# Optimization experiments

Measured on AMD Instinct MI355X. Metric: run time of the kernel, lower is better.

## Reference

```python
import jax, jax.numpy as jnp
import numpy as np

C = 8.0


def setup_inputs() -> dict:
    key = jax.random.key(0)
    k1, k2, k3, k4 = jax.random.split(key, 4)
    B, H, W = 16, 512, 512
    grid = jax.random.normal(k1, (B, 2, H, W), jnp.float32)
    u = jax.random.uniform(k2, (B, 2), jnp.float32)
    # dx = -C*x takes both signs (exercise both branches); dy = C*y >= 0 as the
    # original torch slicing requires.
    gt_sym_axis = jnp.stack([u[:, 0] * 2.0 - 1.0, u[:, 1]], axis=-1)
    gd_sym_axis = jax.random.normal(k3, (B, 2), jnp.float32)
    mask = jax.random.uniform(k4, (B, H, W), jnp.float32)
    return {"grid": grid, "gt_sym_axis": gt_sym_axis,
            "gd_sym_axis": gd_sym_axis, "mask": mask}


def _per_item(g, m, dx, dy, sym_x, sym_y):
    # g: (2, H, W) flow grid, m: (H, W) mask; dx, dy, sym_x, sym_y scalars.
    _, h, w = g.shape
    dy1f = jnp.floor(dy); dx1f = jnp.floor(dx)
    dy2f = dy1f + 1.0;    dx2f = dx1f + 1.0
    dy1 = dy1f.astype(jnp.int32); dy2 = dy1 + 1
    dx1 = dx1f.astype(jnp.int32); dx2 = dx1 + 1

    ii = jnp.arange(h)[:, None]   # (H, 1)
    jj = jnp.arange(w)[None, :]   # (1, W)

    def gat(arr, r, c):
        # clipped dynamic gather; invalid region is masked out later
        return arr[..., jnp.clip(r, 0, h - 1), jnp.clip(c, 0, w - 1)]

    wcol = {1: dx2f - dx, 2: dx - dx1f}   # bilinear col weights (dx1 / dx2)
    wrow = {1: dy2f - dy, 2: dy - dy1f}   # bilinear row weights (dy1 / dy2)
    dys = {1: dy1, 2: dy2}
    dxs = {1: dx1, 2: dx2}

    # ---- dx > 0 branch: delta_ba(i,j) = g[i,j] - g[i+dy_a, j+dx_b] ----
    delta_p = jnp.zeros_like(g)
    for b in (1, 2):
        for a in (1, 2):
            delta_p = delta_p + wcol[b] * wrow[a] * (g - gat(g, ii + dys[a], jj + dxs[b]))
    valid_p = ((ii < h - dy2) & (jj < w - dx2)).astype(g.dtype)
    err_p = delta_p[0] * sym_y + delta_p[1] * sym_x
    cnt_p = ((h - dy2) * (w - dx2)).astype(g.dtype)
    loss_p = jnp.sum(m * valid_p * err_p * err_p) / cnt_p

    # ---- dx <= 0 branch: delta_ba(i,j) = g[i+dy2, j+t_b] - g[i+s_a, j+t_b-dx_b] ----
    s = {1: 1, 2: 0}   # row base offset for dy1 / dy2 variant
    t = {1: 0, 2: 1}   # col base offset for dx1 / dx2 variant
    delta_n = jnp.zeros_like(g)
    for b in (1, 2):
        for a in (1, 2):
            first = gat(g, ii + dy2, jj + t[b])
            second = gat(g, ii + s[a], jj + t[b] - dxs[b])
            delta_n = delta_n + wcol[b] * wrow[a] * (first - second)
    valid_n = ((ii < h - dy2) & (jj < w + dx1)).astype(g.dtype)
    m_n = gat(m, ii + dy2, jj - dx1)
    err_n = delta_n[0] * sym_y + delta_n[1] * sym_x
    cnt_n = ((h - dy2) * (w + dx1)).astype(g.dtype)
    loss_n = jnp.sum(m_n * valid_n * err_n * err_n) / cnt_n

    return jnp.where(dx > 0, loss_p, loss_n)


def reference(grid, gt_sym_axis, gd_sym_axis, mask):
    dx = -C * gt_sym_axis[:, 0]
    dy = C * gt_sym_axis[:, 1]
    sym_x = gd_sym_axis[:, 0]
    sym_y = gd_sym_axis[:, 1]
    losses = jax.vmap(_per_item)(grid, mask, dx, dy, sym_x, sym_y)
    return jnp.mean(losses)
```

## Files before the change

### kernel.cpp

```cpp
#include <hip/hip_runtime.h>

#define HH 512
#define WW 512
#define NB 16
#define NRB 2
#define NCHUNK (HH / NRB)
#define NBLOCKS (NB * NCHUNK)

__device__ __forceinline__ int swz(int c) { return ((c & 3) << 7) | (c >> 2); }

__global__ __launch_bounds__(256) void mbfs_main(
    const float* __restrict__ grid,
    const float* __restrict__ gt,
    const float* __restrict__ gd,
    const float* __restrict__ mask,
    float* __restrict__ partials)
{
    __shared__ float lds[6 * 512];

    const int b    = blockIdx.y;
    const int i0   = blockIdx.x * NRB;
    const int tid  = threadIdx.x;
    const int rsub = tid >> 7;
    const int jt   = tid & 127;
    const int j0   = jt << 2;

    const float dx   = -8.0f * gt[2 * b + 0];
    const float dy   =  8.0f * gt[2 * b + 1];
    const float symx = gd[2 * b + 0];
    const float symy = gd[2 * b + 1];

    const float dy1f = floorf(dy);
    const float dx1f = floorf(dx);
    const int dy1 = (int)dy1f;
    const int dx1 = (int)dx1f;
    const int dy2 = dy1 + 1;
    const int dx2 = dx1 + 1;
    const float wc1 = (dx1f + 1.0f) - dx;
    const float wc2 = dx - dx1f;
    const float wr1 = (dy1f + 1.0f) - dy;
    const float wr2 = dy - dy1f;

    const float* g0 = grid + (size_t)b * 2 * HH * WW;
    const float* g1 = g0 + HH * WW;
    const float* mk = mask + (size_t)b * HH * WW;

    const int imax = HH - dy2;
    float acc = 0.0f;
    float cnt;

    if (dx > 0.0f) {
        const int jmax = WW - dx2;
        cnt = (float)imax * (float)jmax;

        for (int t = tid; t < 6 * 128; t += 256) {
            const int s  = t >> 7;
            const int f  = t & 127;
            const int c  = f << 2;
            const int rr = (s < 3) ? s : s - 3;
            const float* gp = (s < 3) ? g0 : g1;
            int ir = min(i0 + dy1 + rr, HH - 1);
            const float4 v = *(const float4*)(gp + ir * WW + c);
            float* L = lds + s * 512;
            L[swz(c)]     = v.x;
            L[swz(c + 1)] = v.y;
            L[swz(c + 2)] = v.z;
            L[swz(c + 3)] = v.w;
        }
        __syncthreads();

        const int i = i0 + rsub;
        if (i < imax) {
            const float4 c0 = *(const float4*)(g0 + i * WW + j0);
            const float4 c1 = *(const float4*)(g1 + i * WW + j0);
            const float4 mv = *(const float4*)(mk + i * WW + j0);
            const float* A0 = lds + rsub * 512;
            const float* B0 = lds + (rsub + 1) * 512;
            const float* A1 = lds + (3 + rsub) * 512;
            const float* B1 = lds + (4 + rsub) * 512;

            float z0[5], z1[5];
            #pragma unroll
            for (int k = 0; k < 5; ++k) {
                const int c  = min(j0 + dx1 + k, WW - 1);
                const int sc = swz(c);
                z0[k] = wr1 * A0[sc] + wr2 * B0[sc];
                z1[k] = wr1 * A1[sc] + wr2 * B1[sc];
            }
            const float cc0[4] = {c0.x, c0.y, c0.z, c0.w};
            const float cc1[4] = {c1.x, c1.y, c1.z, c1.w};
            const float mm[4]  = {mv.x, mv.y, mv.z, mv.w};
            #pragma unroll
            for (int k = 0; k < 4; ++k) {
                const float s0 = wc1 * z0[k] + wc2 * z0[k + 1];
                const float s1 = wc1 * z1[k] + wc2 * z1[k + 1];
                const float d0 = cc0[k] - s0;
                const float d1 = cc1[k] - s1;
                const float e  = d0 * symy + d1 * symx;
                const float w  = (j0 + k < jmax) ? mm[k] : 0.0f;
                acc += w * e * e;
            }
        }
    } else {
        const int a    = -dx1;
        const int jmax = WW + dx1;
        cnt = (float)imax * (float)jmax;

        for (int t = tid; t < 4 * 128; t += 256) {
            const int s  = t >> 7;
            const int f  = t & 127;
            const int c  = f << 2;
            const int rr = s & 1;
            const float* gp = (s < 2) ? g0 : g1;
            int ir = min(i0 + dy2 + rr, HH - 1);
            const float4 v = *(const float4*)(gp + ir * WW + c);
            float* L = lds + s * 512;
            L[swz(c)]     = v.x;
            L[swz(c + 1)] = v.y;
            L[swz(c + 2)] = v.z;
            L[swz(c + 3)] = v.w;
        }
        __syncthreads();

        const int i = i0 + rsub;
        if (i < imax) {
            const float4 p00 = *(const float4*)(g0 + i * WW + j0);
            const float4 p01 = *(const float4*)(g0 + (i + 1) * WW + j0);
            const float4 p10 = *(const float4*)(g1 + i * WW + j0);
            const float4 p11 = *(const float4*)(g1 + (i + 1) * WW + j0);
            const float4 mv  = *(const float4*)(mk + (i + dy2) * WW + j0);
            const float* H0 = lds + rsub * 512;
            const float* H1 = lds + (2 + rsub) * 512;

            float hh0[5], hh1[5];
            #pragma unroll
            for (int k = 0; k < 5; ++k) {
                int c = j0 - a + k;
                c = max(0, min(c, WW - 1));
                const int sc = swz(c);
                hh0[k] = H0[sc];
                hh1[k] = H1[sc];
            }
            const float q00[4] = {p00.x, p00.y, p00.z, p00.w};
            const float q01[4] = {p01.x, p01.y, p01.z, p01.w};
            const float q10[4] = {p10.x, p10.y, p10.z, p10.w};
            const float q11[4] = {p11.x, p11.y, p11.z, p11.w};
            const float mm[4]  = {mv.x, mv.y, mv.z, mv.w};
            #pragma unroll
            for (int k = 0; k < 4; ++k) {
                const float zn0 = wr1 * q01[k] + wr2 * q00[k];
                const float zn1 = wr1 * q11[k] + wr2 * q10[k];
                const float d0  = wc1 * hh0[k] + wc2 * hh0[k + 1] - zn0;
                const float d1  = wc1 * hh1[k] + wc2 * hh1[k + 1] - zn1;
                const float e   = d0 * symy + d1 * symx;
                const float w   = (j0 + k >= a) ? mm[k] : 0.0f;
                acc += w * e * e;
            }
        }
    }

    #pragma unroll
    for (int off = 32; off > 0; off >>= 1)
        acc += __shfl_down(acc, off, 64);
    __shared__ float part[4];
    const int lane = tid & 63;
    const int wv   = tid >> 6;
    if (lane == 0) part[wv] = acc;
    __syncthreads();
    if (tid == 0) {
        const float s = part[0] + part[1] + part[2] + part[3];
        partials[b * NCHUNK + blockIdx.x] = s / (cnt * (float)NB);
    }
}

__global__ __launch_bounds__(256) void mbfs_reduce(
    const float* __restrict__ partials, float* __restrict__ out)
{
    float v = 0.0f;
    for (int idx = threadIdx.x; idx < NBLOCKS; idx += 256) v += partials[idx];
    #pragma unroll
    for (int off = 32; off > 0; off >>= 1)
        v += __shfl_down(v, off, 64);
    __shared__ float part[4];
    const int lane = threadIdx.x & 63;
    const int wv   = threadIdx.x >> 6;
    if (lane == 0) part[wv] = v;
    __syncthreads();
    if (threadIdx.x == 0) out[0] = part[0] + part[1] + part[2] + part[3];
}

extern "C" void kernel_launch(void* const* d_in, const int* in_sizes, int n_in,
                              void* d_out, int out_size, void* d_ws, size_t ws_size,
                              hipStream_t stream) {
    const float* grid_p = (const float*)d_in[0];
    const float* gt_p   = (const float*)d_in[1];
    const float* gd_p   = (const float*)d_in[2];
    const float* mask_p = (const float*)d_in[3];
    float* out_p = (float*)d_out;
    float* ws_p  = (float*)d_ws;

    dim3 g(NCHUNK, NB);
    mbfs_main<<<g, 256, 0, stream>>>(grid_p, gt_p, gd_p, mask_p, ws_p);
    mbfs_reduce<<<1, 256, 0, stream>>>(ws_p, out_p);
}
```

Before: 97.61 us.

## Replace LDS staging with direct aligned vector loads and process four rows per block

Removes the shared-memory staging of shifted rows and the barrier that follows it. Each thread now reads two aligned float4 windows straight from global memory and selects the shifted elements in registers with a runtime offset. In the dx<=0 branch the indexing is re-based so the shifted operand is the contiguous one, and the mask is read at the shifted position. Each block also handles four rows instead of two, which halves the grid. In exchange, global loads become redundant and overlapping, relying on cache hits, and the register-select logic adds ALU work.

```diff
diff --git a/kernel.cpp b/kernel.cpp
--- a/kernel.cpp
+++ b/kernel.cpp
@@ -3,11 +3,9 @@
 #define HH 512
 #define WW 512
 #define NB 16
-#define NRB 2
+#define NRB 4
 #define NCHUNK (HH / NRB)
 #define NBLOCKS (NB * NCHUNK)
-
-__device__ __forceinline__ int swz(int c) { return ((c & 3) << 7) | (c >> 2); }
 
 __global__ __launch_bounds__(256) void mbfs_main(
     const float* __restrict__ grid,
@@ -16,14 +14,11 @@
     const float* __restrict__ mask,
     float* __restrict__ partials)
 {
-    __shared__ float lds[6 * 512];
-
     const int b    = blockIdx.y;
     const int i0   = blockIdx.x * NRB;
     const int tid  = threadIdx.x;
     const int rsub = tid >> 7;
-    const int jt   = tid & 127;
-    const int j0   = jt << 2;
+    const int j0   = (tid & 127) << 2;
 
     const float dx   = -8.0f * gt[2 * b + 0];
     const float dy   =  8.0f * gt[2 * b + 1];
@@ -52,116 +47,140 @@
     if (dx > 0.0f) {
         const int jmax = WW - dx2;
         cnt = (float)imax * (float)jmax;
-
-        for (int t = tid; t < 6 * 128; t += 256) {
-            const int s  = t >> 7;
-            const int f  = t & 127;
-            const int c  = f << 2;
-            const int rr = (s < 3) ? s : s - 3;
-            const float* gp = (s < 3) ? g0 : g1;
-            int ir = min(i0 + dy1 + rr, HH - 1);
-            const float4 v = *(const float4*)(gp + ir * WW + c);
-            float* L = lds + s * 512;
-            L[swz(c)]     = v.x;
-            L[swz(c + 1)] = v.y;
-            L[swz(c + 2)] = v.z;
-            L[swz(c + 3)] = v.w;
-        }
-        __syncthreads();
-
-        const int i = i0 + rsub;
-        if (i < imax) {
-            const float4 c0 = *(const float4*)(g0 + i * WW + j0);
-            const float4 c1 = *(const float4*)(g1 + i * WW + j0);
-            const float4 mv = *(const float4*)(mk + i * WW + j0);
-            const float* A0 = lds + rsub * 512;
-            const float* B0 = lds + (rsub + 1) * 512;
-            const float* A1 = lds + (3 + rsub) * 512;
-            const float* B1 = lds + (4 + rsub) * 512;
-
-            float z0[5], z1[5];
-            #pragma unroll
-            for (int k = 0; k < 5; ++k) {
-                const int c  = min(j0 + dx1 + k, WW - 1);
-                const int sc = swz(c);
-                z0[k] = wr1 * A0[sc] + wr2 * B0[sc];
-                z1[k] = wr1 * A1[sc] + wr2 * B1[sc];
-            }
-            const float cc0[4] = {c0.x, c0.y, c0.z, c0.w};
-            const float cc1[4] = {c1.x, c1.y, c1.z, c1.w};
-            const float mm[4]  = {mv.x, mv.y, mv.z, mv.w};
-            #pragma unroll
-            for (int k = 0; k < 4; ++k) {
-                const float s0 = wc1 * z0[k] + wc2 * z0[k + 1];
-                const float s1 = wc1 * z1[k] + wc2 * z1[k + 1];
-                const float d0 = cc0[k] - s0;
-                const float d1 = cc1[k] - s1;
-                const float e  = d0 * symy + d1 * symx;
-                const float w  = (j0 + k < jmax) ? mm[k] : 0.0f;
-                acc += w * e * e;
+        const int  b0   = (j0 + dx1) & ~3;
+        const int  base = min(b0, WW - 8);
+        const bool sh   = (b0 != base);
+        const int  off  = dx1 & 3;
+
+        #pragma unroll
+        for (int p = 0; p < 2; ++p) {
+            const int i = i0 + rsub + 2 * p;
+            if (i < imax) {
+                const float4 c0 = *(const float4*)(g0 + i * WW + j0);
+                const float4 c1 = *(const float4*)(g1 + i * WW + j0);
+                const float4 mv = *(const float4*)(mk + i * WW + j0);
+
+                const float* A0 = g0 + (i + dy1) * WW + base;
+                const float* B0 = g0 + (i + dy2) * WW + base;
+                const float* A1 = g1 + (i + dy1) * WW + base;
+                const float* B1 = g1 + (i + dy2) * WW + base;
+                const float4 a0l = *(const float4*)(A0);
+                const float4 a0h = *(const float4*)(A0 + 4);
+                const float4 b0l = *(const float4*)(B0);
+                const float4 b0h = *(const float4*)(B0 + 4);
+                const float4 a1l = *(const float4*)(A1);
+                const float4 a1h = *(const float4*)(A1 + 4);
+                const float4 b1l = *(const float4*)(B1);
+                const float4 b1h = *(const float4*)(B1 + 4);
+
+                const float z0[8] = {
+                    wr1 * a0l.x + wr2 * b0l.x, wr1 * a0l.y + wr2 * b0l.y,
+                    wr1 * a0l.z + wr2 * b0l.z, wr1 * a0l.w + wr2 * b0l.w,
+                    wr1 * a0h.x + wr2 * b0h.x, wr1 * a0h.y + wr2 * b0h.y,
+                    wr1 * a0h.z + wr2 * b0h.z, wr1 * a0h.w + wr2 * b0h.w };
+                const float z1[8] = {
+                    wr1 * a1l.x + wr2 * b1l.x, wr1 * a1l.y + wr2 * b1l.y,
+                    wr1 * a1l.z + wr2 * b1l.z, wr1 * a1l.w + wr2 * b1l.w,
+                    wr1 * a1h.x + wr2 * b1h.x, wr1 * a1h.y + wr2 * b1h.y,
+                    wr1 * a1h.z + wr2 * b1h.z, wr1 * a1h.w + wr2 * b1h.w };
+
+                float y0[5], y1[5];
+                #pragma unroll
+                for (int m = 0; m < 5; ++m) {
+                    const int iu = off + m;
+                    const int is = min(iu + 4, 7);
+                    y0[m] = sh ? z0[is] : z0[iu];
+                    y1[m] = sh ? z1[is] : z1[iu];
+                }
+                const float cc0[4] = {c0.x, c0.y, c0.z, c0.w};
+                const float cc1[4] = {c1.x, c1.y, c1.z, c1.w};
+                const float mm[4]  = {mv.x, mv.y, mv.z, mv.w};
+                #pragma unroll
+                for (int k = 0; k < 4; ++k) {
+                    const float s0 = wc1 * y0[k] + wc2 * y0[k + 1];
+                    const float s1 = wc1 * y1[k] + wc2 * y1[k + 1];
+                    const float d0 = cc0[k] - s0;
+                    const float d1 = cc1[k] - s1;
+                    const float e  = d0 * symy + d1 * symx;
+                    const float w  = (j0 + k < jmax) ? mm[k] : 0.0f;
+                    acc += w * e * e;
+                }
             }
         }
     } else {
         const int a    = -dx1;
-        const int jmax = WW + dx1;
+        const int jmax = WW - a;
         cnt = (float)imax * (float)jmax;
-
-        for (int t = tid; t < 4 * 128; t += 256) {
-            const int s  = t >> 7;
-            const int f  = t & 127;
-            const int c  = f << 2;
-            const int rr = s & 1;
-            const float* gp = (s < 2) ? g0 : g1;
-            int ir = min(i0 + dy2 + rr, HH - 1);
-            const float4 v = *(const float4*)(gp + ir * WW + c);
-            float* L = lds + s * 512;
-            L[swz(c)]     = v.x;
-            L[swz(c + 1)] = v.y;
-            L[swz(c + 2)] = v.z;
-            L[swz(c + 3)] = v.w;
-        }
-        __syncthreads();
-
-        const int i = i0 + rsub;
-        if (i < imax) {
-            const float4 p00 = *(const float4*)(g0 + i * WW + j0);
-            const float4 p01 = *(const float4*)(g0 + (i + 1) * WW + j0);
-            const float4 p10 = *(const float4*)(g1 + i * WW + j0);
-            const float4 p11 = *(const float4*)(g1 + (i + 1) * WW + j0);
-            const float4 mv  = *(const float4*)(mk + (i + dy2) * WW + j0);
-            const float* H0 = lds + rsub * 512;
-            const float* H1 = lds + (2 + rsub) * 512;
-
-            float hh0[5], hh1[5];
-            #pragma unroll
-            for (int k = 0; k < 5; ++k) {
-                int c = j0 - a + k;
-                c = max(0, min(c, WW - 1));
-                const int sc = swz(c);
-                hh0[k] = H0[sc];
-                hh1[k] = H1[sc];
-            }
-            const float q00[4] = {p00.x, p00.y, p00.z, p00.w};
-            const float q01[4] = {p01.x, p01.y, p01.z, p01.w};
-            const float q10[4] = {p10.x, p10.y, p10.z, p10.w};
-            const float q11[4] = {p11.x, p11.y, p11.z, p11.w};
-            const float mm[4]  = {mv.x, mv.y, mv.z, mv.w};
-            #pragma unroll
-            for (int k = 0; k < 4; ++k) {
-                const float zn0 = wr1 * q01[k] + wr2 * q00[k];
-                const float zn1 = wr1 * q11[k] + wr2 * q10[k];
-                const float d0  = wc1 * hh0[k] + wc2 * hh0[k + 1] - zn0;
-                const float d1  = wc1 * hh1[k] + wc2 * hh1[k + 1] - zn1;
-                const float e   = d0 * symy + d1 * symx;
-                const float w   = (j0 + k >= a) ? mm[k] : 0.0f;
-                acc += w * e * e;
+        const int  zb0   = (j0 + a) & ~3;
+        const int  zbase = min(zb0, WW - 8);
+        const bool sh    = (zb0 != zbase);
+        const int  off   = a & 3;
+
+        #pragma unroll
+        for (int p = 0; p < 2; ++p) {
+            const int i = i0 + rsub + 2 * p;
+            if (i < imax) {
+                const float* H0 = g0 + (i + dy2) * WW;
+                const float* H1 = g1 + (i + dy2) * WW;
+                const float4 h04 = *(const float4*)(H0 + j0);
+                const float4 h14 = *(const float4*)(H1 + j0);
+                const int je = min(j0 + 4, WW - 1);
+                const float hh0[5] = {h04.x, h04.y, h04.z, h04.w, H0[je]};
+                const float hh1[5] = {h14.x, h14.y, h14.z, h14.w, H1[je]};
+
+                const float* R0a = g0 + (i + 1) * WW + zbase;
+                const float* R0b = g0 + i * WW + zbase;
+                const float* R1a = g1 + (i + 1) * WW + zbase;
+                const float* R1b = g1 + i * WW + zbase;
+                const float* MM  = mk + (i + dy2) * WW + zbase;
+                const float4 r0al = *(const float4*)(R0a);
+                const float4 r0ah = *(const float4*)(R0a + 4);
+                const float4 r0bl = *(const float4*)(R0b);
+                const float4 r0bh = *(const float4*)(R0b + 4);
+                const float4 r1al = *(const float4*)(R1a);
+                const float4 r1ah = *(const float4*)(R1a + 4);
+                const float4 r1bl = *(const float4*)(R1b);
+                const float4 r1bh = *(const float4*)(R1b + 4);
+                const float4 mml  = *(const float4*)(MM);
+                const float4 mmh  = *(const float4*)(MM + 4);
+
+                const float z0[8] = {
+                    wr1 * r0al.x + wr2 * r0bl.x, wr1 * r0al.y + wr2 * r0bl.y,
+                    wr1 * r0al.z + wr2 * r0bl.z, wr1 * r0al.w + wr2 * r0bl.w,
+                    wr1 * r0ah.x + wr2 * r0bh.x, wr1 * r0ah.y + wr2 * r0bh.y,
+                    wr1 * r0ah.z + wr2 * r0bh.z, wr1 * r0ah.w + wr2 * r0bh.w };
+                const float z1[8] = {
+                    wr1 * r1al.x + wr2 * r1bl.x, wr1 * r1al.y + wr2 * r1bl.y,
+                    wr1 * r1al.z + wr2 * r1bl.z, wr1 * r1al.w + wr2 * r1bl.w,
+                    wr1 * r1ah.x + wr2 * r1bh.x, wr1 * r1ah.y + wr2 * r1bh.y,
+                    wr1 * r1ah.z + wr2 * r1bh.z, wr1 * r1ah.w + wr2 * r1bh.w };
+                const float zm[8] = {mml.x, mml.y, mml.z, mml.w,
+                                     mmh.x, mmh.y, mmh.z, mmh.w};
+
+                float y0[4], y1[4], ym[4];
+                #pragma unroll
+                for (int m = 0; m < 4; ++m) {
+                    const int iu = off + m;
+                    const int is = min(iu + 4, 7);
+                    y0[m] = sh ? z0[is] : z0[iu];
+                    y1[m] = sh ? z1[is] : z1[iu];
+                    ym[m] = sh ? zm[is] : zm[iu];
+                }
+                #pragma unroll
+                for (int k = 0; k < 4; ++k) {
+                    const float d0 = wc1 * hh0[k] + wc2 * hh0[k + 1] - y0[k];
+                    const float d1 = wc1 * hh1[k] + wc2 * hh1[k + 1] - y1[k];
+                    const float e  = d0 * symy + d1 * symx;
+                    const float w  = (j0 + k < jmax) ? ym[k] : 0.0f;
+                    acc += w * e * e;
+                }
             }
         }
     }
 
     #pragma unroll
-    for (int off = 32; off > 0; off >>= 1)
-        acc += __shfl_down(acc, off, 64);
+    for (int offr = 32; offr > 0; offr >>= 1)
+        acc += __shfl_down(acc, offr, 64);
     __shared__ float part[4];
     const int lane = tid & 63;
     const int wv   = tid >> 6;
```

Measured after the change: 93.17 us. 4.6% less time.
